# Performance work log

Measured on AMD Instinct MI355X. Metric: run time of the kernel, lower is better.

## Reference

```python
import jax, jax.numpy as jnp
import numpy as np

NT, NS, NH, NG, NR, NC = 365, 300, 128, 32, 8, 1


def _linear_params(key, fin, fout):
    k1, k2 = jax.random.split(key)
    s = 1.0 / np.sqrt(fin)
    W = jax.random.uniform(k1, (fout, fin), minval=-s, maxval=s, dtype=jnp.float32)
    b = jax.random.uniform(k2, (fout,), minval=-s, maxval=s, dtype=jnp.float32)
    return W, b


def setup_inputs() -> dict:
    key = jax.random.key(0)
    ks = jax.random.split(key, 9)
    x = jax.random.normal(ks[0], (NT, NS, 6), dtype=jnp.float32)
    xc = jax.random.normal(ks[1], (NS, NG), dtype=jnp.float32)
    fcR_w1, fcR_b1 = _linear_params(ks[2], NG, 256)
    fcR_w2, fcR_b2 = _linear_params(ks[3], 256, NH * NR)
    fcW_w1, fcW_b1 = _linear_params(ks[4], NG, 256)
    fcW_w2, fcW_b2 = _linear_params(ks[5], 256, NH * 7)
    fcT_w1, fcT_b1 = _linear_params(ks[6], 6 + NG, 256)
    fcT_w2, fcT_b2 = _linear_params(ks[7], 256, NH * 3)
    fcCT_w, fcCT_b = _linear_params(ks[8], 2 + NG, NC * NH * 3)
    return dict(x=x, xc=xc,
                fcR_w1=fcR_w1, fcR_b1=fcR_b1, fcR_w2=fcR_w2, fcR_b2=fcR_b2,
                fcW_w1=fcW_w1, fcW_b1=fcW_b1, fcW_w2=fcW_w2, fcW_b2=fcW_b2,
                fcT_w1=fcT_w1, fcT_b1=fcT_b1, fcT_w2=fcT_w2, fcT_b2=fcT_b2,
                fcCT_w=fcCT_w, fcCT_b=fcCT_b)


def _mlp(x, w1, b1, w2, b2):
    # Linear -> Tanh -> Dropout(identity in eval) -> Linear
    h = jnp.tanh(x @ w1.T + b1)
    return h @ w2.T + b2


def _conv_ts(q, r):
    # q: [nt, ns, nh]; r: [ns, nh, nr] routing weights. Causal temporal conv:
    # out[t] = sum_i q[t-i] * r[..., i]  (zero padded on the left)
    nt = q.shape[0]
    nr = r.shape[-1]
    qp = jnp.concatenate([jnp.zeros((nr - 1,) + q.shape[1:], q.dtype), q], axis=0)
    out = qp[nr - 1: nr - 1 + nt] * r[None, :, :, 0]
    for i in range(1, nr):
        out = out + qp[nr - 1 - i: nr - 1 - i + nt] * r[None, :, :, i]
    return out


def reference(x, xc, fcR_w1, fcR_b1, fcR_w2, fcR_b2,
              fcW_w1, fcW_b1, fcW_w2, fcW_b2,
              fcT_w1, fcT_b1, fcT_w2, fcT_b2,
              fcCT_w, fcCT_b):
    nh, nr = NH, NR
    P, E, T1, T2 = x[..., 0], x[..., 1], x[..., 2], x[..., 3]
    nt, ns = P.shape
    xcT = jnp.broadcast_to(xc[None], (nt, ns, xc.shape[-1]))
    xT = jnp.concatenate([x, xcT], axis=-1)                      # [nt, ns, 6+ng]

    # static gates per (site, bucket): sepPar with ['sigmoid']*4,'exp','relu','skip'
    w = _mlp(xc, fcW_w1, fcW_b1, fcW_w2, fcW_b2)                 # [ns, nh*7]
    kp = jax.nn.sigmoid(w[:, 0 * nh:1 * nh])
    ks_ = jax.nn.sigmoid(w[:, 1 * nh:2 * nh])
    kg = jax.nn.sigmoid(w[:, 2 * nh:3 * nh])
    gp = jax.nn.sigmoid(w[:, 3 * nh:4 * nh])
    gL = jnp.exp(w[:, 4 * nh:5 * nh]) * 2.0
    qb = jax.nn.relu(w[:, 5 * nh:6 * nh])
    ga = jax.nn.softmax(w[:, 6 * nh:7 * nh], axis=1)             # [ns, nh]

    # time-varying gates: ['skip','relu','exp']; vi overridden by hardsigmoid(v*2)
    v = _mlp(xT, fcT_w1, fcT_b1, fcT_w2, fcT_b2)                 # [nt, ns, nh*3]
    vi = jnp.clip(v[:, :, :nh] * 2.0 / 6.0 + 0.5, 0.0, 1.0)     # F.hardsigmoid(v*2)
    ve = jax.nn.relu(v[:, :, nh:2 * nh]) * 2.0
    vm = jnp.exp(v[:, :, 2 * nh:3 * nh])

    wR = _mlp(xc, fcR_w1, fcR_b1, fcR_w2, fcR_b2)                # [ns, nh*nr]
    r = jax.nn.relu(wR[:, :nh * nr]).reshape(ns, nh, nr)

    # snow fraction vf = arccos((T1+T2)/(T2-T1))/3.1415, overridden at extremes
    denom = T2 - T1
    ratio = jnp.clip((T1 + T2) / jnp.where(denom == 0, 1.0, denom), -1.0, 1.0)
    vf = jnp.arccos(ratio) / 3.1415
    vf = jnp.where(T1 >= 0, 0.0, jnp.where(T2 <= 0, 1.0, vf))
    Ps = P * vf                                                  # snow  [nt, ns]
    Pl = (P * (1.0 - vf))[:, :, None] * vi                       # rain  [nt, ns, nh]
    Ev = E[:, :, None] * ve                                      # evap  [nt, ns, nh]

    def step(carry, inp):
        Sf, Ss, Sg = carry
        Ps_k, Pl_k, Ev_k, vm_k = inp
        qf = jnp.minimum(Sf + Ps_k, vm_k)
        Sf = jax.nn.relu(Sf + Ps_k - vm_k)
        H = jax.nn.relu(Ss + Pl_k + qf - Ev_k)
        qp_ = jax.nn.relu(kp * (H - gL))
        qs = ks_ * jnp.minimum(H, gL)
        Ss = H - qp_ - qs
        qso = qs * (1.0 - gp)
        qsg = qs * gp
        qg = kg * (Sg + qsg) + qb
        Sg = (1.0 - kg) * (Sg + qsg) - qb
        return (Sf, Ss, Sg), (qp_, qso, qg)

    z = jnp.zeros((ns, nh), dtype=x.dtype)
    _, (Q1T, Q2T, Q3T) = jax.lax.scan(step, (z, z, z),
                                      (Ps[:, :, None], Pl, Ev, vm))

    Q1R = _conv_ts(Q1T, r)
    Q2R = _conv_ts(Q2T, r)
    Q3R = _conv_ts(Q3T, r)
    outQ = jnp.sum((Q1R + Q2R + Q3R) * ga, axis=2)               # [nt, ns]

    xTc = jnp.concatenate([T1[:, :, None], T2[:, :, None], xcT], axis=-1)
    wC = xTc @ fcCT_w.T + fcCT_b                                 # [nt, ns, nh*3]
    cp = jnp.exp(wC[:, :, 0 * nh:1 * nh])
    cs = jnp.exp(wC[:, :, 1 * nh:2 * nh])
    cg = jnp.exp(wC[:, :, 2 * nh:3 * nh])
    C1R = _conv_ts(Q1T * cp / 10.0, r)
    C2R = _conv_ts(Q2T * cs, r)
    C3R = _conv_ts(Q3T * cg, r)
    outC = jnp.sum((C1R + C2R + C3R) * ga, axis=2) / outQ
    return outQ, outC
```

## Files before the change

kernel.cpp:

```cpp
#include <hip/hip_runtime.h>
#include <math.h>

#define NTT 365
#define NSS 300
#define NROWS (NTT*NSS)
#define TPAD 384

using bf16x8 = __attribute__((ext_vector_type(8))) short;
using f32x4  = __attribute__((ext_vector_type(4))) float;

__device__ __forceinline__ float sigf(float v) { return 1.0f / (1.0f + __expf(-v)); }

__device__ __forceinline__ float tanhfast(float x) {
    float e = __expf(2.0f * x);
    return 1.0f - 2.0f * __builtin_amdgcn_rcpf(1.0f + e);
}

__device__ __forceinline__ unsigned short f2bf(float f) {
    unsigned u = __builtin_bit_cast(unsigned, f);
    u += 0x7FFFu + ((u >> 16) & 1u);
    return (unsigned short)(u >> 16);
}

__global__ __launch_bounds__(256) void k_prep(const float* __restrict__ w1,
                                              const float* __restrict__ w2,
                                              unsigned short* __restrict__ w1s,
                                              unsigned short* __restrict__ w2s)
{
    int G = blockIdx.x * 256 + threadIdx.x;
    if (G < 2048) {
        int lane = G & 63, ks = (G >> 6) & 1, tile = G >> 7;
        int o = tile * 16 + (lane & 15);
        int kb = ks * 32 + (lane >> 4) * 8;
        unsigned short tmp[8];
#pragma unroll
        for (int e = 0; e < 8; ++e) {
            int k = kb + e;
            tmp[e] = (k < 38) ? f2bf(w1[o * 38 + k]) : (unsigned short)0;
        }
        *(bf16x8*)(w1s + (size_t)G * 8) = *(bf16x8*)tmp;
    } else if (G < 2048 + 12288) {
        int G2 = G - 2048;
        int lane = G2 & 63, ks = (G2 >> 6) & 7, tile = G2 >> 9;
        int o = tile * 16 + (lane & 15);
        int kb = ks * 32 + (lane >> 4) * 8;
        unsigned short tmp[8];
#pragma unroll
        for (int e = 0; e < 8; ++e) tmp[e] = f2bf(w2[o * 256 + kb + e]);
        *(bf16x8*)(w2s + (size_t)G2 * 8) = *(bf16x8*)tmp;
    }
}

__global__ __launch_bounds__(256) void k_site(
    const float* __restrict__ xc,
    const float* __restrict__ wW1, const float* __restrict__ bW1,
    const float* __restrict__ wW2, const float* __restrict__ bW2,
    const float* __restrict__ wR1, const float* __restrict__ bR1,
    const float* __restrict__ wR2, const float* __restrict__ bR2,
    float* __restrict__ wsite, float* __restrict__ rsite)
{
    __shared__ float xcb[10][32];
    __shared__ float hW[10][256];
    __shared__ float hR[10][256];
    int tid = threadIdx.x;
    int s0 = blockIdx.x * 10;
    int os = blockIdx.y;
    for (int i = tid; i < 10 * 32; i += 256) xcb[i / 32][i % 32] = xc[s0 * 32 + i];
    __syncthreads();
    {
        int j = tid;
        float aW[10], aR[10];
#pragma unroll
        for (int r = 0; r < 10; ++r) { aW[r] = bW1[j]; aR[r] = bR1[j]; }
        for (int k = 0; k < 32; ++k) {
            float wv = wW1[j * 32 + k], rv = wR1[j * 32 + k];
#pragma unroll
            for (int r = 0; r < 10; ++r) { float xv = xcb[r][k]; aW[r] += xv * wv; aR[r] += xv * rv; }
        }
#pragma unroll
        for (int r = 0; r < 10; ++r) { hW[r][j] = tanhfast(aW[r]); hR[r][j] = tanhfast(aR[r]); }
    }
    __syncthreads();
    if (tid < 240) {
        int o_lin = os * 240 + tid;
        float acc[10];
        if (o_lin < 896) {
            int o = o_lin;
#pragma unroll
            for (int r = 0; r < 10; ++r) acc[r] = bW2[o];
            for (int k = 0; k < 256; ++k) {
                float wv = wW2[o * 256 + k];
#pragma unroll
                for (int r = 0; r < 10; ++r) acc[r] += hW[r][k] * wv;
            }
#pragma unroll
            for (int r = 0; r < 10; ++r) wsite[(s0 + r) * 896 + o] = acc[r];
        } else {
            int o = o_lin - 896;
#pragma unroll
            for (int r = 0; r < 10; ++r) acc[r] = bR2[o];
            for (int k = 0; k < 256; ++k) {
                float wv = wR2[o * 256 + k];
#pragma unroll
                for (int r = 0; r < 10; ++r) acc[r] += hR[r][k] * wv;
            }
#pragma unroll
            for (int r = 0; r < 10; ++r) rsite[(s0 + r) * 1024 + o] = acc[r];
        }
    }
}

__global__ __launch_bounds__(128) void k_softmax_ga(const float* __restrict__ wsite,
                                                    float* __restrict__ ga)
{
    int s = blockIdx.x, tid = threadIdx.x;
    __shared__ float red[2];
    float v = wsite[s * 896 + 6 * 128 + tid];
    float m = v;
#pragma unroll
    for (int off = 32; off >= 1; off >>= 1) m = fmaxf(m, __shfl_xor(m, off));
    if ((tid & 63) == 0) red[tid >> 6] = m;
    __syncthreads();
    m = fmaxf(red[0], red[1]);
    __syncthreads();
    float e = __expf(v - m);
    float ssum = e;
#pragma unroll
    for (int off = 32; off >= 1; off >>= 1) ssum += __shfl_xor(ssum, off);
    if ((tid & 63) == 0) red[tid >> 6] = ssum;
    __syncthreads();
    ssum = red[0] + red[1];
    ga[s * 128 + tid] = e / ssum;
}

__global__ __launch_bounds__(512) void k_fcT(
    const float* __restrict__ x, const float* __restrict__ xc,
    const unsigned short* __restrict__ w1s, const float* __restrict__ b1,
    const unsigned short* __restrict__ w2s, const float* __restrict__ b2,
    float4* __restrict__ PT, unsigned* __restrict__ NVu)
{
    __shared__ unsigned short A1[64][72];
    __shared__ unsigned short hb[64][264];
    __shared__ float2 pfE[64];
    int tid = threadIdx.x;
    int row0 = blockIdx.x * 64;

    for (int idx = tid; idx < 64 * 64; idx += 512) {
        int r = idx >> 6, c = idx & 63;
        int g = row0 + r;
        float val = 0.0f;
        if (g < NROWS) {
            if (c < 6) val = x[g * 6 + c];
            else if (c < 38) { int s = g % NSS; val = xc[s * 32 + (c - 6)]; }
        }
        A1[r][c] = f2bf(val);
    }
    if (tid < 64) {
        int r = tid, g = row0 + r;
        float P = 0, E = 0, T1 = 0, T2 = 0;
        if (g < NROWS) { P = x[g * 6]; E = x[g * 6 + 1]; T1 = x[g * 6 + 2]; T2 = x[g * 6 + 3]; }
        float den = T2 - T1;
        float dg = (den == 0.0f) ? 1.0f : den;
        float ratio = fminf(fmaxf((T1 + T2) / dg, -1.0f), 1.0f);
        float vf = acosf(ratio) * (1.0f / 3.1415f);
        vf = (T1 >= 0.0f) ? 0.0f : ((T2 <= 0.0f) ? 1.0f : vf);
        pfE[r] = make_float2(P * (1.0f - vf), 2.0f * E);
        if (g < NROWS) PT[g] = make_float4(P * vf, T1, T2, vf);
    }
    __syncthreads();

    int lane = tid & 63, wv = tid >> 6;
    int r16 = lane & 15;
    int kg = (lane >> 4) * 8;
    int rq = (lane >> 4) * 4;

    {
        int mt = wv & 3, nb = (wv >> 2) * 8;
        f32x4 acc[8];
#pragma unroll
        for (int i = 0; i < 8; ++i) acc[i] = (f32x4){0.f, 0.f, 0.f, 0.f};
#pragma unroll
        for (int ks = 0; ks < 2; ++ks) {
            bf16x8 a = *(const bf16x8*)&A1[mt * 16 + r16][ks * 32 + kg];
#pragma unroll
            for (int i = 0; i < 8; ++i) {
                bf16x8 b = *(const bf16x8*)(w1s + ((size_t)(((nb + i) * 2 + ks) * 64 + lane) << 3));
                acc[i] = __builtin_amdgcn_mfma_f32_16x16x32_bf16(a, b, acc[i], 0, 0, 0);
            }
        }
#pragma unroll
        for (int i = 0; i < 8; ++i) {
            int col = (nb + i) * 16 + r16;
            float bias = b1[col];
#pragma unroll
            for (int j = 0; j < 4; ++j) {
                int row = mt * 16 + rq + j;
                hb[row][col] = f2bf(tanhfast(acc[i][j] + bias));
            }
        }
    }
    __syncthreads();

    {
        int t0 = wv, t1 = wv + 8, t2 = wv + 16;
        f32x4 acc[4][3];
#pragma unroll
        for (int m = 0; m < 4; ++m)
#pragma unroll
            for (int c = 0; c < 3; ++c) acc[m][c] = (f32x4){0.f, 0.f, 0.f, 0.f};
#pragma unroll
        for (int ks = 0; ks < 8; ++ks) {
            bf16x8 b0 = *(const bf16x8*)(w2s + ((size_t)((t0 * 8 + ks) * 64 + lane) << 3));
            bf16x8 b1v = *(const bf16x8*)(w2s + ((size_t)((t1 * 8 + ks) * 64 + lane) << 3));
            bf16x8 b2v = *(const bf16x8*)(w2s + ((size_t)((t2 * 8 + ks) * 64 + lane) << 3));
#pragma unroll
            for (int m = 0; m < 4; ++m) {
                bf16x8 a = *(const bf16x8*)&hb[m * 16 + r16][ks * 32 + kg];
                acc[m][0] = __builtin_amdgcn_mfma_f32_16x16x32_bf16(a, b0, acc[m][0], 0, 0, 0);
                acc[m][1] = __builtin_amdgcn_mfma_f32_16x16x32_bf16(a, b1v, acc[m][1], 0, 0, 0);
                acc[m][2] = __builtin_amdgcn_mfma_f32_16x16x32_bf16(a, b2v, acc[m][2], 0, 0, 0);
            }
        }
        int hcol = wv * 16 + r16;
        float bias0 = b2[hcol], bias1 = b2[128 + hcol], bias2 = b2[256 + hcol];
#pragma unroll
        for (int m = 0; m < 4; ++m) {
            float2 pf[4];
#pragma unroll
            for (int j = 0; j < 4; ++j) pf[j] = pfE[m * 16 + rq + j];
#pragma unroll
            for (int j = 0; j < 4; ++j) {
                int r = m * 16 + rq + j;
                int g = row0 + r;
                if (g < NROWS) {
                    float vi = fminf(fmaxf((acc[m][0][j] + bias0) * (1.0f / 3.0f) + 0.5f, 0.0f), 1.0f);
                    float pl = pf[j].x * vi;
                    float ev = pf[j].y * fmaxf(acc[m][1][j] + bias1, 0.0f);
                    float vmv = __expf(acc[m][2][j] + bias2);
                    unsigned pk = (unsigned)f2bf(pl - ev) | ((unsigned)f2bf(vmv) << 16);
                    NVu[(size_t)g * 128 + hcol] = pk;
                }
            }
        }
    }
}

__global__ __launch_bounds__(64) void k_scan(
    const float* __restrict__ xc,
    const float* __restrict__ wsite, const float* __restrict__ rsite,
    const float* __restrict__ gaw,
    const float* __restrict__ ctw, const float* __restrict__ ctb,
    const float4* __restrict__ PTg, const unsigned* __restrict__ NVu,
    float* __restrict__ pQ, float* __restrict__ pC)
{
    __shared__ float4 ptlds[TPAD];
    __shared__ __align__(16) float red[16][68];
    int lane = threadIdx.x;
    int b = blockIdx.x;
    int s = b >> 1, half = b & 1;
    int h = half * 64 + lane;

    for (int t = lane; t < TPAD; t += 64) ptlds[t] = PTg[(size_t)t * NSS + s];

    const float* wrow = wsite + s * 896;
    float kp = sigf(wrow[0 * 128 + h]);
    float ks = sigf(wrow[1 * 128 + h]);
    float kg = sigf(wrow[2 * 128 + h]);
    float gp = sigf(wrow[3 * 128 + h]);
    float gpc = 1.0f - gp;
    float gL = __expf(wrow[4 * 128 + h]) * 2.0f;
    float kpgl = kp * gL;
    float qb = fmaxf(wrow[5 * 128 + h], 0.0f);
    float ga = gaw[s * 128 + h];
    float rt0 = fmaxf(rsite[s * 1024 + h * 8 + 0], 0.0f) * ga;
    float rt1 = fmaxf(rsite[s * 1024 + h * 8 + 1], 0.0f) * ga;
    float rt2 = fmaxf(rsite[s * 1024 + h * 8 + 2], 0.0f) * ga;
    float rt3 = fmaxf(rsite[s * 1024 + h * 8 + 3], 0.0f) * ga;
    float rt4 = fmaxf(rsite[s * 1024 + h * 8 + 4], 0.0f) * ga;
    float rt5 = fmaxf(rsite[s * 1024 + h * 8 + 5], 0.0f) * ga;
    float rt6 = fmaxf(rsite[s * 1024 + h * 8 + 6], 0.0f) * ga;
    float rt7 = fmaxf(rsite[s * 1024 + h * 8 + 7], 0.0f) * ga;
    const float L2E = 1.4426950408889634f;
    const float LG01 = -3.3219280948873623f;
    float cpw0, cpw1, cpb, csw0, csw1, csb, cgw0, cgw1, cgb;
    {
        const float* wr = ctw + (0 * 128 + h) * 34;
        float base = ctb[0 * 128 + h];
        for (int k = 0; k < 32; ++k) base += wr[2 + k] * xc[s * 32 + k];
        cpw0 = wr[0] * L2E; cpw1 = wr[1] * L2E; cpb = base * L2E + LG01;
    }
    {
        const float* wr = ctw + (1 * 128 + h) * 34;
        float base = ctb[1 * 128 + h];
        for (int k = 0; k < 32; ++k) base += wr[2 + k] * xc[s * 32 + k];
        csw0 = wr[0] * L2E; csw1 = wr[1] * L2E; csb = base * L2E;
    }
    {
        const float* wr = ctw + (2 * 128 + h) * 34;
        float base = ctb[2 * 128 + h];
        for (int k = 0; k < 32; ++k) base += wr[2 + k] * xc[s * 32 + k];
        cgw0 = wr[0] * L2E; cgw1 = wr[1] * L2E; cgb = base * L2E;
    }
    float Sf = 0.0f, Ss = 0.0f, Sg = 0.0f;
    float q0 = 0, q1 = 0, q2 = 0, q3 = 0, q4 = 0, q5 = 0, q6 = 0, q7 = 0;
    float c0 = 0, c1 = 0, c2 = 0, c3 = 0, c4 = 0, c5 = 0, c6 = 0, c7 = 0;

    const unsigned* nvbase = NVu + (size_t)s * 128 + h;
    unsigned nv[16];
#pragma unroll
    for (int i = 0; i < 16; ++i) nv[i] = nvbase[(size_t)i * NSS * 128];

    float4 pt[4];
#pragma unroll
    for (int i = 0; i < 4; ++i) pt[i] = ptlds[i];

    auto reduce8 = [&](int base) {
        int v = lane >> 2, sub = lane & 3;
        const float4* rp = (const float4*)&red[v][0];
        float4 a0 = rp[sub * 4 + 0];
        float4 a1 = rp[sub * 4 + 1];
        float4 a2 = rp[sub * 4 + 2];
        float4 a3 = rp[sub * 4 + 3];
        float sA = (a0.x + a0.y) + (a0.z + a0.w);
        float sB = (a1.x + a1.y) + (a1.z + a1.w);
        float sC = (a2.x + a2.y) + (a2.z + a2.w);
        float sD = (a3.x + a3.y) + (a3.z + a3.w);
        float sm = (sA + sB) + (sC + sD);
        sm += __shfl_xor(sm, 1);
        sm += __shfl_xor(sm, 2);
        int t = base + (v & 7);
        if (sub == 0 && t < NTT) {
            float* bp = (v < 8) ? pQ : pC;
            bp[((size_t)t * NSS + s) * 2 + half] = sm;
        }
    };

    for (int tb = 0; tb < 368; tb += 16) {
#pragma unroll
        for (int u = 0; u < 16; ++u) {
            int t = tb + u;
            unsigned nvu = nv[u];
            float net = __builtin_bit_cast(float, nvu << 16);
            float vm  = __builtin_bit_cast(float, nvu & 0xFFFF0000u);
            nv[u] = nvbase[(size_t)(t + 16) * NSS * 128];
            float psv = pt[u & 3].x, T1 = pt[u & 3].y, T2 = pt[u & 3].z;
            pt[u & 3] = ptlds[t + 4];
            float t1v = Sf + psv;
            float qf = fminf(t1v, vm);
            Sf = fmaxf(t1v - vm, 0.0f);
            float H = fmaxf(Ss + qf + net, 0.0f);
            float qp = fmaxf(kp * H - kpgl, 0.0f);
            float qs = ks * fminf(H, gL);
            Ss = H - qp - qs;
            float qso = qs * gpc;
            float qsg = qs * gp;
            float tg = Sg + qsg;
            float qg = kg * tg + qb;
            Sg = tg - qg;
            float cp = exp2f(cpw0 * T1 + cpw1 * T2 + cpb);
            float cs = exp2f(csw0 * T1 + csw1 * T2 + csb);
            float cg = exp2f(cgw0 * T1 + cgw1 * T2 + cgb);
            float QS = qp + qso + qg;
            float CS = qp * cp + qso * cs + qg * cg;
            q0 += QS * rt0; q1 += QS * rt1; q2 += QS * rt2; q3 += QS * rt3;
            q4 += QS * rt4; q5 += QS * rt5; q6 += QS * rt6; q7 += QS * rt7;
            c0 += CS * rt0; c1 += CS * rt1; c2 += CS * rt2; c3 += CS * rt3;
            c4 += CS * rt4; c5 += CS * rt5; c6 += CS * rt6; c7 += CS * rt7;
            red[u & 7][lane] = q0;
            red[8 + (u & 7)][lane] = c0;
            q0 = q1; q1 = q2; q2 = q3; q3 = q4; q4 = q5; q5 = q6; q6 = q7; q7 = 0.0f;
            c0 = c1; c1 = c2; c2 = c3; c3 = c4; c4 = c5; c5 = c6; c6 = c7; c7 = 0.0f;
            if (u == 7) reduce8(tb);
            if (u == 15) reduce8(tb + 8);
        }
    }
}

__global__ __launch_bounds__(256) void k_final(const float* __restrict__ pQ,
                                               const float* __restrict__ pC,
                                               float* __restrict__ out)
{
    int i = blockIdx.x * 256 + threadIdx.x;
    if (i < NROWS) {
        float q = pQ[i * 2] + pQ[i * 2 + 1];
        float c = pC[i * 2] + pC[i * 2 + 1];
        out[i] = q;
        out[NROWS + i] = c / q;
    }
}

extern "C" void kernel_launch(void* const* d_in, const int* in_sizes, int n_in,
                              void* d_out, int out_size, void* d_ws, size_t ws_size,
                              hipStream_t stream)
{
    const float* x      = (const float*)d_in[0];
    const float* xc     = (const float*)d_in[1];
    const float* fcR_w1 = (const float*)d_in[2];
    const float* fcR_b1 = (const float*)d_in[3];
    const float* fcR_w2 = (const float*)d_in[4];
    const float* fcR_b2 = (const float*)d_in[5];
    const float* fcW_w1 = (const float*)d_in[6];
    const float* fcW_b1 = (const float*)d_in[7];
    const float* fcW_w2 = (const float*)d_in[8];
    const float* fcW_b2 = (const float*)d_in[9];
    const float* fcT_w1 = (const float*)d_in[10];
    const float* fcT_b1 = (const float*)d_in[11];
    const float* fcT_w2 = (const float*)d_in[12];
    const float* fcT_b2 = (const float*)d_in[13];
    const float* fcCT_w = (const float*)d_in[14];
    const float* fcCT_b = (const float*)d_in[15];
    float* out = (float*)d_out;

    float* ws = (float*)d_ws;
    size_t o_w    = 0;
    size_t o_r    = o_w  + 300 * 896;
    size_t o_ga   = o_r  + 300 * 1024;
    size_t o_PT   = o_ga + 300 * 128;
    size_t o_NV   = o_PT + (size_t)TPAD * NSS * 4;
    size_t o_pQ   = o_NV + (size_t)TPAD * NSS * 128;
    size_t o_pC   = o_pQ + (size_t)NROWS * 2;
    size_t o_w1bf = o_pC + (size_t)NROWS * 2;
    size_t o_w2bf = o_w1bf + 8192;

    float* wsite = ws + o_w;
    float* rsite = ws + o_r;
    float* gaw   = ws + o_ga;
    float4* PT   = (float4*)(ws + o_PT);
    unsigned* NVu = (unsigned*)(ws + o_NV);
    float* pQ    = ws + o_pQ;
    float* pC    = ws + o_pC;
    unsigned short* w1s = (unsigned short*)(ws + o_w1bf);
    unsigned short* w2s = (unsigned short*)(ws + o_w2bf);

    k_prep<<<56, 256, 0, stream>>>(fcT_w1, fcT_w2, w1s, w2s);
    k_site<<<dim3(30, 8), 256, 0, stream>>>(xc, fcW_w1, fcW_b1, fcW_w2, fcW_b2,
                                            fcR_w1, fcR_b1, fcR_w2, fcR_b2, wsite, rsite);
    k_softmax_ga<<<300, 128, 0, stream>>>(wsite, gaw);
    int nblk2 = (NROWS + 63) / 64;
    k_fcT<<<nblk2, 512, 0, stream>>>(x, xc, w1s, fcT_b1, w2s, fcT_b2, PT, NVu);
    k_scan<<<600, 64, 0, stream>>>(xc, wsite, rsite, gaw, fcCT_w, fcCT_b,
                                   PT, NVu, pQ, pC);
    k_final<<<(NROWS + 255) / 256, 256, 0, stream>>>(pQ, pC, out);
}
```

Before: 161.5 us.

## Split scan into Q and C role blocks and precompute concentration coefficients

The scan kernel now launches twice as many single-wave blocks. Each block takes one role: either the discharge accumulation (Q) or the concentration accumulation (C, with the exp2 terms). The recurrence is computed redundantly in both roles, so each wave carries half the accumulators and register pressure drops. On a 256-CU device, 600 waves left much of the machine idle. The per-site fcCT dot products move into a separate k_ct kernel, and the LDS reduction is simplified to a single 8-row buffer. The cost is duplicated recurrence work and doubled NV/PT memory reads.

```diff
diff --git a/kernel.cpp b/kernel.cpp
--- a/kernel.cpp
+++ b/kernel.cpp
@@ -131,6 +131,37 @@
     __syncthreads();
     ssum = red[0] + red[1];
     ga[s * 128 + tid] = e / ssum;
+}
+
+__global__ __launch_bounds__(128) void k_ct(const float* __restrict__ xc,
+                                            const float* __restrict__ ctw,
+                                            const float* __restrict__ ctb,
+                                            float* __restrict__ ctp8,
+                                            float* __restrict__ ctpb)
+{
+    __shared__ float xcs[32];
+    int s = blockIdx.x, h = threadIdx.x;
+    if (h < 32) xcs[h] = xc[s * 32 + h];
+    __syncthreads();
+    const float L2E = 1.4426950408889634f;
+    const float LG01 = -3.3219280948873623f;
+    float out[8];
+    float cgb = 0.0f;
+#pragma unroll
+    for (int g = 0; g < 3; ++g) {
+        const float* wr = ctw + (g * 128 + h) * 34;
+        float base = ctb[g * 128 + h];
+        for (int k = 0; k < 32; ++k) base += wr[2 + k] * xcs[k];
+        float w0 = wr[0] * L2E, w1 = wr[1] * L2E;
+        float bb = base * L2E + ((g == 0) ? LG01 : 0.0f);
+        if (g == 0) { out[0] = w0; out[1] = w1; out[2] = bb; }
+        else if (g == 1) { out[3] = w0; out[4] = w1; out[5] = bb; }
+        else { out[6] = w0; out[7] = w1; cgb = bb; }
+    }
+    float4* dst = (float4*)(ctp8 + ((size_t)s * 128 + h) * 8);
+    dst[0] = make_float4(out[0], out[1], out[2], out[3]);
+    dst[1] = make_float4(out[4], out[5], out[6], out[7]);
+    ctpb[(size_t)s * 128 + h] = cgb;
 }
 
 __global__ __launch_bounds__(512) void k_fcT(
@@ -245,95 +276,24 @@
     }
 }
 
-__global__ __launch_bounds__(64) void k_scan(
-    const float* __restrict__ xc,
-    const float* __restrict__ wsite, const float* __restrict__ rsite,
-    const float* __restrict__ gaw,
-    const float* __restrict__ ctw, const float* __restrict__ ctb,
-    const float4* __restrict__ PTg, const unsigned* __restrict__ NVu,
-    float* __restrict__ pQ, float* __restrict__ pC)
-{
-    __shared__ float4 ptlds[TPAD];
-    __shared__ __align__(16) float red[16][68];
-    int lane = threadIdx.x;
-    int b = blockIdx.x;
-    int s = b >> 1, half = b & 1;
-    int h = half * 64 + lane;
-
-    for (int t = lane; t < TPAD; t += 64) ptlds[t] = PTg[(size_t)t * NSS + s];
-
-    const float* wrow = wsite + s * 896;
-    float kp = sigf(wrow[0 * 128 + h]);
-    float ks = sigf(wrow[1 * 128 + h]);
-    float kg = sigf(wrow[2 * 128 + h]);
-    float gp = sigf(wrow[3 * 128 + h]);
-    float gpc = 1.0f - gp;
-    float gL = __expf(wrow[4 * 128 + h]) * 2.0f;
-    float kpgl = kp * gL;
-    float qb = fmaxf(wrow[5 * 128 + h], 0.0f);
-    float ga = gaw[s * 128 + h];
-    float rt0 = fmaxf(rsite[s * 1024 + h * 8 + 0], 0.0f) * ga;
-    float rt1 = fmaxf(rsite[s * 1024 + h * 8 + 1], 0.0f) * ga;
-    float rt2 = fmaxf(rsite[s * 1024 + h * 8 + 2], 0.0f) * ga;
-    float rt3 = fmaxf(rsite[s * 1024 + h * 8 + 3], 0.0f) * ga;
-    float rt4 = fmaxf(rsite[s * 1024 + h * 8 + 4], 0.0f) * ga;
-    float rt5 = fmaxf(rsite[s * 1024 + h * 8 + 5], 0.0f) * ga;
-    float rt6 = fmaxf(rsite[s * 1024 + h * 8 + 6], 0.0f) * ga;
-    float rt7 = fmaxf(rsite[s * 1024 + h * 8 + 7], 0.0f) * ga;
-    const float L2E = 1.4426950408889634f;
-    const float LG01 = -3.3219280948873623f;
-    float cpw0, cpw1, cpb, csw0, csw1, csb, cgw0, cgw1, cgb;
-    {
-        const float* wr = ctw + (0 * 128 + h) * 34;
-        float base = ctb[0 * 128 + h];
-        for (int k = 0; k < 32; ++k) base += wr[2 + k] * xc[s * 32 + k];
-        cpw0 = wr[0] * L2E; cpw1 = wr[1] * L2E; cpb = base * L2E + LG01;
-    }
-    {
-        const float* wr = ctw + (1 * 128 + h) * 34;
-        float base = ctb[1 * 128 + h];
-        for (int k = 0; k < 32; ++k) base += wr[2 + k] * xc[s * 32 + k];
-        csw0 = wr[0] * L2E; csw1 = wr[1] * L2E; csb = base * L2E;
-    }
-    {
-        const float* wr = ctw + (2 * 128 + h) * 34;
-        float base = ctb[2 * 128 + h];
-        for (int k = 0; k < 32; ++k) base += wr[2 + k] * xc[s * 32 + k];
-        cgw0 = wr[0] * L2E; cgw1 = wr[1] * L2E; cgb = base * L2E;
-    }
+template<int ROLE>
+__device__ __forceinline__ void scan_loop(
+    int lane, int s, int half,
+    float kp, float ks, float kg, float gp, float gpc, float gL, float kpgl, float qb,
+    float r0, float r1, float r2, float r3, float r4, float r5, float r6, float r7,
+    float cpw0, float cpw1, float cpb, float csw0, float csw1, float csb,
+    float cgw0, float cgw1, float cgb,
+    const unsigned* __restrict__ nvbase, const float4* ptlds, float (*red)[68],
+    float* __restrict__ outp)
+{
     float Sf = 0.0f, Ss = 0.0f, Sg = 0.0f;
-    float q0 = 0, q1 = 0, q2 = 0, q3 = 0, q4 = 0, q5 = 0, q6 = 0, q7 = 0;
-    float c0 = 0, c1 = 0, c2 = 0, c3 = 0, c4 = 0, c5 = 0, c6 = 0, c7 = 0;
-
-    const unsigned* nvbase = NVu + (size_t)s * 128 + h;
+    float a0 = 0, a1 = 0, a2 = 0, a3 = 0, a4 = 0, a5 = 0, a6 = 0, a7 = 0;
     unsigned nv[16];
 #pragma unroll
     for (int i = 0; i < 16; ++i) nv[i] = nvbase[(size_t)i * NSS * 128];
-
     float4 pt[4];
 #pragma unroll
     for (int i = 0; i < 4; ++i) pt[i] = ptlds[i];
-
-    auto reduce8 = [&](int base) {
-        int v = lane >> 2, sub = lane & 3;
-        const float4* rp = (const float4*)&red[v][0];
-        float4 a0 = rp[sub * 4 + 0];
-        float4 a1 = rp[sub * 4 + 1];
-        float4 a2 = rp[sub * 4 + 2];
-        float4 a3 = rp[sub * 4 + 3];
-        float sA = (a0.x + a0.y) + (a0.z + a0.w);
-        float sB = (a1.x + a1.y) + (a1.z + a1.w);
-        float sC = (a2.x + a2.y) + (a2.z + a2.w);
-        float sD = (a3.x + a3.y) + (a3.z + a3.w);
-        float sm = (sA + sB) + (sC + sD);
-        sm += __shfl_xor(sm, 1);
-        sm += __shfl_xor(sm, 2);
-        int t = base + (v & 7);
-        if (sub == 0 && t < NTT) {
-            float* bp = (v < 8) ? pQ : pC;
-            bp[((size_t)t * NSS + s) * 2 + half] = sm;
-        }
-    };
 
     for (int tb = 0; tb < 368; tb += 16) {
 #pragma unroll
@@ -357,22 +317,87 @@
             float tg = Sg + qsg;
             float qg = kg * tg + qb;
             Sg = tg - qg;
-            float cp = exp2f(cpw0 * T1 + cpw1 * T2 + cpb);
-            float cs = exp2f(csw0 * T1 + csw1 * T2 + csb);
-            float cg = exp2f(cgw0 * T1 + cgw1 * T2 + cgb);
-            float QS = qp + qso + qg;
-            float CS = qp * cp + qso * cs + qg * cg;
-            q0 += QS * rt0; q1 += QS * rt1; q2 += QS * rt2; q3 += QS * rt3;
-            q4 += QS * rt4; q5 += QS * rt5; q6 += QS * rt6; q7 += QS * rt7;
-            c0 += CS * rt0; c1 += CS * rt1; c2 += CS * rt2; c3 += CS * rt3;
-            c4 += CS * rt4; c5 += CS * rt5; c6 += CS * rt6; c7 += CS * rt7;
-            red[u & 7][lane] = q0;
-            red[8 + (u & 7)][lane] = c0;
-            q0 = q1; q1 = q2; q2 = q3; q3 = q4; q4 = q5; q5 = q6; q6 = q7; q7 = 0.0f;
-            c0 = c1; c1 = c2; c2 = c3; c3 = c4; c4 = c5; c5 = c6; c6 = c7; c7 = 0.0f;
-            if (u == 7) reduce8(tb);
-            if (u == 15) reduce8(tb + 8);
-        }
+            float val;
+            if (ROLE == 0) {
+                val = qp + qso + qg;
+            } else {
+                float cp = exp2f(cpw0 * T1 + cpw1 * T2 + cpb);
+                float cs = exp2f(csw0 * T1 + csw1 * T2 + csb);
+                float cg = exp2f(cgw0 * T1 + cgw1 * T2 + cgb);
+                val = qp * cp + qso * cs + qg * cg;
+            }
+            a0 += val * r0; a1 += val * r1; a2 += val * r2; a3 += val * r3;
+            a4 += val * r4; a5 += val * r5; a6 += val * r6; a7 += val * r7;
+            red[u & 7][lane] = a0;
+            a0 = a1; a1 = a2; a2 = a3; a3 = a4; a4 = a5; a5 = a6; a6 = a7; a7 = 0.0f;
+            if (u == 7 || u == 15) {
+                int base = tb + ((u == 7) ? 0 : 8);
+                int v = lane >> 3, sub = lane & 7;
+                const float4* rp4 = (const float4*)&red[v][0];
+                float4 b0 = rp4[sub * 2], b1 = rp4[sub * 2 + 1];
+                float sm = ((b0.x + b0.y) + (b0.z + b0.w)) + ((b1.x + b1.y) + (b1.z + b1.w));
+                sm += __shfl_xor(sm, 1);
+                sm += __shfl_xor(sm, 2);
+                sm += __shfl_xor(sm, 4);
+                int tt = base + v;
+                if (sub == 0 && tt < NTT) outp[((size_t)tt * NSS + s) * 2 + half] = sm;
+            }
+        }
+    }
+}
+
+__global__ __launch_bounds__(64) void k_scan(
+    const float* __restrict__ wsite, const float* __restrict__ rsite,
+    const float* __restrict__ gaw,
+    const float* __restrict__ ctp8, const float* __restrict__ ctpb,
+    const float4* __restrict__ PTg, const unsigned* __restrict__ NVu,
+    float* __restrict__ pQ, float* __restrict__ pC)
+{
+    __shared__ float4 ptlds[TPAD];
+    __shared__ __align__(16) float red[8][68];
+    int lane = threadIdx.x;
+    int b = blockIdx.x;
+    int role = b & 1;
+    int half = (b >> 1) & 1;
+    int s = b >> 2;
+    int h = half * 64 + lane;
+
+    for (int t = lane; t < TPAD; t += 64) ptlds[t] = PTg[(size_t)t * NSS + s];
+
+    const float* wrow = wsite + s * 896;
+    float kp = sigf(wrow[0 * 128 + h]);
+    float ks = sigf(wrow[1 * 128 + h]);
+    float kg = sigf(wrow[2 * 128 + h]);
+    float gp = sigf(wrow[3 * 128 + h]);
+    float gpc = 1.0f - gp;
+    float gL = __expf(wrow[4 * 128 + h]) * 2.0f;
+    float kpgl = kp * gL;
+    float qb = fmaxf(wrow[5 * 128 + h], 0.0f);
+    float ga = gaw[s * 128 + h];
+    float r0 = fmaxf(rsite[s * 1024 + h * 8 + 0], 0.0f) * ga;
+    float r1 = fmaxf(rsite[s * 1024 + h * 8 + 1], 0.0f) * ga;
+    float r2 = fmaxf(rsite[s * 1024 + h * 8 + 2], 0.0f) * ga;
+    float r3 = fmaxf(rsite[s * 1024 + h * 8 + 3], 0.0f) * ga;
+    float r4 = fmaxf(rsite[s * 1024 + h * 8 + 4], 0.0f) * ga;
+    float r5 = fmaxf(rsite[s * 1024 + h * 8 + 5], 0.0f) * ga;
+    float r6 = fmaxf(rsite[s * 1024 + h * 8 + 6], 0.0f) * ga;
+    float r7 = fmaxf(rsite[s * 1024 + h * 8 + 7], 0.0f) * ga;
+
+    const unsigned* nvbase = NVu + (size_t)s * 128 + h;
+
+    if (role == 0) {
+        scan_loop<0>(lane, s, half, kp, ks, kg, gp, gpc, gL, kpgl, qb,
+                     r0, r1, r2, r3, r4, r5, r6, r7,
+                     0.f, 0.f, 0.f, 0.f, 0.f, 0.f, 0.f, 0.f, 0.f,
+                     nvbase, ptlds, red, pQ);
+    } else {
+        const float4* cp4 = (const float4*)(ctp8 + ((size_t)s * 128 + h) * 8);
+        float4 c0 = cp4[0], c1 = cp4[1];
+        float cgb = ctpb[(size_t)s * 128 + h];
+        scan_loop<1>(lane, s, half, kp, ks, kg, gp, gpc, gL, kpgl, qb,
+                     r0, r1, r2, r3, r4, r5, r6, r7,
+                     c0.x, c0.y, c0.z, c0.w, c1.x, c1.y, c1.z, c1.w, cgb,
+                     nvbase, ptlds, red, pC);
     }
 }
 
@@ -421,6 +446,8 @@
     size_t o_pC   = o_pQ + (size_t)NROWS * 2;
     size_t o_w1bf = o_pC + (size_t)NROWS * 2;
     size_t o_w2bf = o_w1bf + 8192;
+    size_t o_ctp  = o_w2bf + 49152;
+    size_t o_ctpb = o_ctp + (size_t)300 * 128 * 8;
 
     float* wsite = ws + o_w;
     float* rsite = ws + o_r;
@@ -431,14 +458,17 @@
     float* pC    = ws + o_pC;
     unsigned short* w1s = (unsigned short*)(ws + o_w1bf);
     unsigned short* w2s = (unsigned short*)(ws + o_w2bf);
+    float* ctp8  = ws + o_ctp;
+    float* ctpb  = ws + o_ctpb;
 
     k_prep<<<56, 256, 0, stream>>>(fcT_w1, fcT_w2, w1s, w2s);
     k_site<<<dim3(30, 8), 256, 0, stream>>>(xc, fcW_w1, fcW_b1, fcW_w2, fcW_b2,
                                             fcR_w1, fcR_b1, fcR_w2, fcR_b2, wsite, rsite);
     k_softmax_ga<<<300, 128, 0, stream>>>(wsite, gaw);
+    k_ct<<<300, 128, 0, stream>>>(xc, fcCT_w, fcCT_b, ctp8, ctpb);
     int nblk2 = (NROWS + 63) / 64;
     k_fcT<<<nblk2, 512, 0, stream>>>(x, xc, w1s, fcT_b1, w2s, fcT_b2, PT, NVu);
-    k_scan<<<600, 64, 0, stream>>>(xc, wsite, rsite, gaw, fcCT_w, fcCT_b,
-                                   PT, NVu, pQ, pC);
+    k_scan<<<1200, 64, 0, stream>>>(wsite, rsite, gaw, ctp8, ctpb,
+                                    PT, NVu, pQ, pC);
     k_final<<<(NROWS + 255) / 256, 256, 0, stream>>>(pQ, pC, out);
 }
```

Result: slower. 178.6 us (+10.6%).
